# Optimization experiments

Measured on AMD Instinct MI355X. Metric: run time of the kernel, lower is better.

## Reference

```python
import jax, jax.numpy as jnp
import numpy as np

B, N_DIM, K_DIM = 16384, 4096, 128


def setup_inputs() -> dict:
    key = jax.random.key(0)
    k1, k2, k3, k4 = jax.random.split(key, 4)
    x = jax.random.normal(k1, (B, N_DIM), dtype=jnp.float32)
    # nn.Linear(n_dim, 1): weight (1, n_dim), bias (1,)
    lim = 1.0 / np.sqrt(N_DIM)
    W = jax.random.uniform(k2, (1, N_DIM), dtype=jnp.float32, minval=-lim, maxval=lim)
    b = jax.random.uniform(k3, (1,), dtype=jnp.float32, minval=-lim, maxval=lim)
    # V initialized N(0, 0.001)
    V = 0.001 * jax.random.normal(k4, (N_DIM, K_DIM), dtype=jnp.float32)
    return {"x": x, "W": W, "b": b, "V": V}


def reference(x, W, b, V):
    # linear part: (B,1)
    linear = x @ W.T + b
    # term1 = 0.5 * sum_k (x @ V)_k^2  (torch code's 'sum_of_square')
    xv = x @ V  # (B, k)
    term1 = 0.5 * jnp.sum(xv * xv, axis=1, keepdims=True)
    # term2: torch's expand+matmul+bmm reduces algebraically to
    # -0.5 * (sum_i x_i)^2 * ||V.sum(0)||^2  (identical math, no (B,n,n) tensor)
    s = jnp.sum(V, axis=0)  # (k,)
    xsum = jnp.sum(x, axis=1, keepdims=True)  # (B,1)
    term2 = -0.5 * (xsum * xsum) * jnp.dot(s, s)
    return linear + term1 + term2
```

## Files before the change

kernel.cpp:

```cpp
#include <hip/hip_runtime.h>

typedef __bf16 bf16;
typedef __bf16 bf16x8 __attribute__((ext_vector_type(8)));
typedef float f32x16 __attribute__((ext_vector_type(16)));

#define B_ROWS 16384
#define N_DIM  4096
#define K_DIM  128

__global__ __launch_bounds__(256) void prep_kernel(const float* __restrict__ V,
                                                   float* __restrict__ spart,
                                                   bf16* __restrict__ Ut) {
    __shared__ bf16 tile[128 * 136];
    __shared__ float sp[256];
    const int t = threadIdx.x;
    const int jbase = blockIdx.x * 128;
    const int c  = t & 127;
    const int j0 = t >> 7;

    float sacc = 0.f;
#pragma unroll 8
    for (int i = 0; i < 64; ++i) {
        int j = j0 + 2 * i;
        float v = V[(size_t)(jbase + j) * K_DIM + c];
        sacc += v;
        tile[c * 136 + j] = (bf16)v;
    }
    sp[t] = sacc;
    __syncthreads();
    if (t < 128) spart[blockIdx.x * 128 + t] = sp[t] + sp[t + 128];

    const int col = t >> 1, half = t & 1;
#pragma unroll
    for (int i = 0; i < 4; ++i) {
        uint4 d = *(const uint4*)&tile[col * 136 + half * 64 + i * 16];
        *(uint4*)&Ut[(size_t)col * N_DIM + jbase + half * 64 + i * 16] = d;
    }
}

__global__ __launch_bounds__(128) void finalize_s(const float* __restrict__ spart,
                                                  float* __restrict__ snorm_out) {
    const int t = threadIdx.x;
    float s = 0.f;
#pragma unroll
    for (int b = 0; b < 32; ++b) s += spart[b * 128 + t];
    float sq = s * s;
#pragma unroll
    for (int m = 32; m >= 1; m >>= 1) sq += __shfl_down(sq, m, 64);
    __shared__ float red[2];
    if ((t & 63) == 0) red[t >> 6] = sq;
    __syncthreads();
    if (t == 0) snorm_out[0] = red[0] + red[1];
}

__global__ __launch_bounds__(256, 2) void fm_main(const float* __restrict__ x,
                                                  const float* __restrict__ W,
                                                  const float* __restrict__ bptr,
                                                  const bf16* __restrict__ Ut,
                                                  const float* __restrict__ snorm_ptr,
                                                  float* __restrict__ out) {
    __shared__ bf16  xs[2][32 * 72];
    __shared__ bf16  us[2][128 * 64];
    __shared__ float redxs[256];
    __shared__ float redxw[256];
    __shared__ float rowsq[4 * 32];

    const int t    = threadIdx.x;
    const int wave = t >> 6;
    const int lane = t & 63;
    const int l31  = lane & 31;
    const int h    = lane >> 5;
    const int r0   = blockIdx.x * 32;

    const int srow = t >> 3;
    const int scg  = t & 7;

    f32x16 acc;
#pragma unroll
    for (int i = 0; i < 16; ++i) acc[i] = 0.f;

    float xsum_acc = 0.f, xw_acc = 0.f;
    const float* xrow = x + (size_t)(r0 + srow) * N_DIM + scg * 8;
    const float* wrow = W + scg * 8;
    const bf16* ub = Ut + (size_t)(wave * 32 + (lane >> 3)) * N_DIM + (lane & 7) * 8;

    float4 a0 = *(const float4*)(xrow);
    float4 a1 = *(const float4*)(xrow + 4);
    float4 w0 = *(const float4*)(wrow);
    float4 w1 = *(const float4*)(wrow + 4);
#pragma unroll
    for (int j = 0; j < 4; ++j) {
        __builtin_amdgcn_global_load_lds(
            (const __attribute__((address_space(1))) void*)(ub + (size_t)j * 8 * N_DIM),
            (__attribute__((address_space(3))) void*)&us[0][(wave * 32 + j * 8) * 64],
            16, 0, 0);
    }

    for (int it = 0; it < 64; ++it) {
        const int b = it & 1;
        const int kb_next = (it < 63) ? (it + 1) * 64 : 0;

        bf16x8 xb;
        xb[0] = (bf16)a0.x; xb[1] = (bf16)a0.y; xb[2] = (bf16)a0.z; xb[3] = (bf16)a0.w;
        xb[4] = (bf16)a1.x; xb[5] = (bf16)a1.y; xb[6] = (bf16)a1.z; xb[7] = (bf16)a1.w;
        *(bf16x8*)&xs[b][srow * 72 + scg * 8] = xb;

        __syncthreads();

        float4 na0 = *(const float4*)(xrow + kb_next);
        float4 na1 = *(const float4*)(xrow + kb_next + 4);
        float4 nw0 = *(const float4*)(wrow + kb_next);
        float4 nw1 = *(const float4*)(wrow + kb_next + 4);
#pragma unroll
        for (int j = 0; j < 4; ++j) {
            __builtin_amdgcn_global_load_lds(
                (const __attribute__((address_space(1))) void*)(ub + (size_t)j * 8 * N_DIM + kb_next),
                (__attribute__((address_space(3))) void*)&us[b ^ 1][(wave * 32 + j * 8) * 64],
                16, 0, 0);
        }

        xsum_acc += (a0.x + a0.y + a0.z + a0.w) + (a1.x + a1.y + a1.z + a1.w);
        xw_acc   += a0.x * w0.x + a0.y * w0.y + a0.z * w0.z + a0.w * w0.w
                  + a1.x * w1.x + a1.y * w1.y + a1.z * w1.z + a1.w * w1.w;

#pragma unroll
        for (int ks = 0; ks < 64; ks += 16) {
            bf16x8 af  = *(const bf16x8*)&xs[b][l31 * 72 + ks + h * 8];
            bf16x8 bfv = *(const bf16x8*)&us[b][(wave * 32 + l31) * 64 + ks + h * 8];
            acc = __builtin_amdgcn_mfma_f32_32x32x16_bf16(af, bfv, acc, 0, 0, 0);
        }

        a0 = na0; a1 = na1; w0 = nw0; w1 = nw1;
    }

    redxs[t] = xsum_acc;
    redxw[t] = xw_acc;

#pragma unroll
    for (int r = 0; r < 16; ++r) {
        float s = acc[r] * acc[r];
        s += __shfl_xor(s, 1);
        s += __shfl_xor(s, 2);
        s += __shfl_xor(s, 4);
        s += __shfl_xor(s, 8);
        s += __shfl_xor(s, 16);
        if (l31 == 0) {
            int row = (r & 3) + 8 * (r >> 2) + 4 * h;
            rowsq[wave * 32 + row] = s;
        }
    }
    __syncthreads();

    if (t < 32) {
        float xsum = 0.f, xw = 0.f;
#pragma unroll
        for (int g = 0; g < 8; ++g) { xsum += redxs[t * 8 + g]; xw += redxw[t * 8 + g]; }
        float sq = rowsq[t] + rowsq[32 + t] + rowsq[64 + t] + rowsq[96 + t];
        float snorm = snorm_ptr[0];
        float bv = bptr[0];
        out[r0 + t] = bv + xw + 0.5f * sq - 0.5f * xsum * xsum * snorm;
    }
}

extern "C" void kernel_launch(void* const* d_in, const int* in_sizes, int n_in,
                              void* d_out, int out_size, void* d_ws, size_t ws_size,
                              hipStream_t stream) {
    const float* x  = (const float*)d_in[0];
    const float* W  = (const float*)d_in[1];
    const float* bp = (const float*)d_in[2];
    const float* V  = (const float*)d_in[3];
    float* out = (float*)d_out;

    char* ws = (char*)d_ws;
    float* snorm = (float*)ws;
    float* spart = (float*)(ws + 1024);
    bf16*  Ut    = (bf16*)(ws + 32768);

    hipLaunchKernelGGL(prep_kernel, dim3(32), dim3(256), 0, stream, V, spart, Ut);
    hipLaunchKernelGGL(finalize_s, dim3(1), dim3(128), 0, stream, spart, snorm);
    hipLaunchKernelGGL(fm_main, dim3(512), dim3(256), 0, stream, x, W, bp, Ut, snorm, out);
}
```

Measured before the change: 397.9 us.

## Prefetch x two stages ahead, manual barriers, fold finalize kernel into main

The x/W register prefetch now runs two iterations ahead, and __syncthreads is replaced with an explicit lgkmcnt wait, raw s_barrier and sched_barriers. A partial vmcnt wait lets outstanding x loads overlap the MFMA block, which also runs at raised wave priority. The separate finalize_s launch is removed: every fm_main block recomputes the ||sum V||^2 reduction from spart in its epilogue, saving one kernel launch at the cost of redundant per-block work and more registers. The hand-written vmcnt(12) count depends on the exact load ordering the compiler emits.

```diff
diff --git a/kernel.cpp b/kernel.cpp
--- a/kernel.cpp
+++ b/kernel.cpp
@@ -38,32 +38,18 @@
     }
 }
 
-__global__ __launch_bounds__(128) void finalize_s(const float* __restrict__ spart,
-                                                  float* __restrict__ snorm_out) {
-    const int t = threadIdx.x;
-    float s = 0.f;
-#pragma unroll
-    for (int b = 0; b < 32; ++b) s += spart[b * 128 + t];
-    float sq = s * s;
-#pragma unroll
-    for (int m = 32; m >= 1; m >>= 1) sq += __shfl_down(sq, m, 64);
-    __shared__ float red[2];
-    if ((t & 63) == 0) red[t >> 6] = sq;
-    __syncthreads();
-    if (t == 0) snorm_out[0] = red[0] + red[1];
-}
-
 __global__ __launch_bounds__(256, 2) void fm_main(const float* __restrict__ x,
                                                   const float* __restrict__ W,
                                                   const float* __restrict__ bptr,
                                                   const bf16* __restrict__ Ut,
-                                                  const float* __restrict__ snorm_ptr,
+                                                  const float* __restrict__ spart,
                                                   float* __restrict__ out) {
     __shared__ bf16  xs[2][32 * 72];
     __shared__ bf16  us[2][128 * 64];
     __shared__ float redxs[256];
     __shared__ float redxw[256];
     __shared__ float rowsq[4 * 32];
+    __shared__ float snred[2];
 
     const int t    = threadIdx.x;
     const int wave = t >> 6;
@@ -84,10 +70,6 @@
     const float* wrow = W + scg * 8;
     const bf16* ub = Ut + (size_t)(wave * 32 + (lane >> 3)) * N_DIM + (lane & 7) * 8;
 
-    float4 a0 = *(const float4*)(xrow);
-    float4 a1 = *(const float4*)(xrow + 4);
-    float4 w0 = *(const float4*)(wrow);
-    float4 w1 = *(const float4*)(wrow + 4);
 #pragma unroll
     for (int j = 0; j < 4; ++j) {
         __builtin_amdgcn_global_load_lds(
@@ -95,42 +77,61 @@
             (__attribute__((address_space(3))) void*)&us[0][(wave * 32 + j * 8) * 64],
             16, 0, 0);
     }
+    float4 a0 = *(const float4*)(xrow);
+    float4 a1 = *(const float4*)(xrow + 4);
+    float4 w0 = *(const float4*)(wrow);
+    float4 w1 = *(const float4*)(wrow + 4);
+    float4 b0 = *(const float4*)(xrow + 64);
+    float4 b1 = *(const float4*)(xrow + 68);
+    float4 v0 = *(const float4*)(wrow + 64);
+    float4 v1 = *(const float4*)(wrow + 68);
 
     for (int it = 0; it < 64; ++it) {
-        const int b = it & 1;
-        const int kb_next = (it < 63) ? (it + 1) * 64 : 0;
+        const int bsel = it & 1;
+        const int kb1 = (it < 63) ? (it + 1) * 64 : 0;
+        const int kb2 = (it < 62) ? (it + 2) * 64 : 0;
 
         bf16x8 xb;
         xb[0] = (bf16)a0.x; xb[1] = (bf16)a0.y; xb[2] = (bf16)a0.z; xb[3] = (bf16)a0.w;
         xb[4] = (bf16)a1.x; xb[5] = (bf16)a1.y; xb[6] = (bf16)a1.z; xb[7] = (bf16)a1.w;
-        *(bf16x8*)&xs[b][srow * 72 + scg * 8] = xb;
+        *(bf16x8*)&xs[bsel][srow * 72 + scg * 8] = xb;
 
-        __syncthreads();
+        asm volatile("s_waitcnt lgkmcnt(0)" ::: "memory");
+        __builtin_amdgcn_s_barrier();
+        __builtin_amdgcn_sched_barrier(0);
 
-        float4 na0 = *(const float4*)(xrow + kb_next);
-        float4 na1 = *(const float4*)(xrow + kb_next + 4);
-        float4 nw0 = *(const float4*)(wrow + kb_next);
-        float4 nw1 = *(const float4*)(wrow + kb_next + 4);
 #pragma unroll
         for (int j = 0; j < 4; ++j) {
             __builtin_amdgcn_global_load_lds(
-                (const __attribute__((address_space(1))) void*)(ub + (size_t)j * 8 * N_DIM + kb_next),
-                (__attribute__((address_space(3))) void*)&us[b ^ 1][(wave * 32 + j * 8) * 64],
+                (const __attribute__((address_space(1))) void*)(ub + (size_t)j * 8 * N_DIM + kb1),
+                (__attribute__((address_space(3))) void*)&us[bsel ^ 1][(wave * 32 + j * 8) * 64],
                 16, 0, 0);
         }
+        __builtin_amdgcn_sched_barrier(0);
+
+        float4 n0 = *(const float4*)(xrow + kb2);
+        float4 n1 = *(const float4*)(xrow + kb2 + 4);
+        float4 m0 = *(const float4*)(wrow + kb2);
+        float4 m1 = *(const float4*)(wrow + kb2 + 4);
 
         xsum_acc += (a0.x + a0.y + a0.z + a0.w) + (a1.x + a1.y + a1.z + a1.w);
         xw_acc   += a0.x * w0.x + a0.y * w0.y + a0.z * w0.z + a0.w * w0.w
                   + a1.x * w1.x + a1.y * w1.y + a1.z * w1.z + a1.w * w1.w;
 
+        asm volatile("s_waitcnt vmcnt(12)" ::: "memory");
+        __builtin_amdgcn_sched_barrier(0);
+
+        __builtin_amdgcn_s_setprio(1);
 #pragma unroll
         for (int ks = 0; ks < 64; ks += 16) {
-            bf16x8 af  = *(const bf16x8*)&xs[b][l31 * 72 + ks + h * 8];
-            bf16x8 bfv = *(const bf16x8*)&us[b][(wave * 32 + l31) * 64 + ks + h * 8];
+            bf16x8 af  = *(const bf16x8*)&xs[bsel][l31 * 72 + ks + h * 8];
+            bf16x8 bfv = *(const bf16x8*)&us[bsel][(wave * 32 + l31) * 64 + ks + h * 8];
             acc = __builtin_amdgcn_mfma_f32_32x32x16_bf16(af, bfv, acc, 0, 0, 0);
         }
+        __builtin_amdgcn_s_setprio(0);
 
-        a0 = na0; a1 = na1; w0 = nw0; w1 = nw1;
+        a0 = b0; a1 = b1; w0 = v0; w1 = v1;
+        b0 = n0; b1 = n1; v0 = m0; v1 = m1;
     }
 
     redxs[t] = xsum_acc;
@@ -149,6 +150,16 @@
             rowsq[wave * 32 + row] = s;
         }
     }
+
+    if (t < 128) {
+        float sv = 0.f;
+#pragma unroll
+        for (int bb = 0; bb < 32; ++bb) sv += spart[bb * 128 + t];
+        float sq = sv * sv;
+#pragma unroll
+        for (int m = 32; m >= 1; m >>= 1) sq += __shfl_down(sq, m, 64);
+        if ((t & 63) == 0) snred[t >> 6] = sq;
+    }
     __syncthreads();
 
     if (t < 32) {
@@ -156,7 +167,7 @@
 #pragma unroll
         for (int g = 0; g < 8; ++g) { xsum += redxs[t * 8 + g]; xw += redxw[t * 8 + g]; }
         float sq = rowsq[t] + rowsq[32 + t] + rowsq[64 + t] + rowsq[96 + t];
-        float snorm = snorm_ptr[0];
+        float snorm = snred[0] + snred[1];
         float bv = bptr[0];
         out[r0 + t] = bv + xw + 0.5f * sq - 0.5f * xsum * xsum * snorm;
     }
@@ -172,11 +183,9 @@
     float* out = (float*)d_out;
 
     char* ws = (char*)d_ws;
-    float* snorm = (float*)ws;
     float* spart = (float*)(ws + 1024);
     bf16*  Ut    = (bf16*)(ws + 32768);
 
     hipLaunchKernelGGL(prep_kernel, dim3(32), dim3(256), 0, stream, V, spart, Ut);
-    hipLaunchKernelGGL(finalize_s, dim3(1), dim3(128), 0, stream, spart, snorm);
-    hipLaunchKernelGGL(fm_main, dim3(512), dim3(256), 0, stream, x, W, bp, Ut, snorm, out);
+    hipLaunchKernelGGL(fm_main, dim3(512), dim3(256), 0, stream, x, W, bp, Ut, spart, out);
 }
```

Result: no change. 397.0 us (-0.2%).
